# Performance work log

Measured on AMD Instinct MI355X. Metric: run time of the kernel, lower is better.

## Reference

```python
import jax, jax.numpy as jnp
import numpy as np

N, E = 200_000, 1_000_000
WIDTH, NUM_HEAD = 128, 8
WN, WA = 1, 1            # width_norm, width_act
C = WIDTH * WN           # pre/norm channels
A = WIDTH * WA           # gate/value channels
BOND_SIZE, BAG = 33, 3
EPS = 1e-5               # GroupNorm eps (torch default)


def group_norm(x, groups, eps=EPS):
    # x: [E, C]; normalize per sample per group (affine=False, spatial size 1)
    e, c = x.shape
    xg = x.reshape(e, groups, c // groups)
    m = xg.mean(-1, keepdims=True)
    v = ((xg - m) ** 2).mean(-1, keepdims=True)
    return ((xg - m) * jax.lax.rsqrt(v + eps)).reshape(e, c)


def grouped1x1(x, w, groups):
    # grouped Conv1d with kernel 1, no bias. x: [E, Cin], w: [Cout, Cin//groups]
    e, cin = x.shape
    cout = w.shape[0]
    xg = x.reshape(e, groups, cin // groups)
    wg = w.reshape(groups, cout // groups, cin // groups)
    return jnp.einsum('egi,goi->ego', xg, wg).reshape(e, cout)


def setup_inputs() -> dict:
    key = jax.random.key(0)
    ks = jax.random.split(key, 12)
    x = jax.random.normal(ks[0], (N, WIDTH), jnp.float32)
    # degrees clamped to >= 1 in the original model
    deg = jnp.floor(jax.random.uniform(ks[1], (N,), jnp.float32, 1.0, 8.0))
    edge_idx = jax.random.randint(ks[2], (2, E), 0, N)
    edge_attr = jax.random.randint(ks[3], (E, BAG), 0, BOND_SIZE)
    s_in = 1.0 / np.sqrt(WIDTH)
    s_g = 1.0 / np.sqrt(C // NUM_HEAD)
    s_p = 1.0 / np.sqrt(A)
    pre0_w = jax.random.normal(ks[4], (C, WIDTH), jnp.float32) * s_in
    pre0_b = jnp.zeros((C,), jnp.float32)
    pre1_w = jax.random.normal(ks[5], (C, WIDTH), jnp.float32) * s_in
    pre1_b = jnp.zeros((C,), jnp.float32)
    emb = jax.random.normal(ks[6], (BOND_SIZE, C), jnp.float32)
    emb = emb.at[0].set(0.0)  # padding_idx=0
    gate_w = jax.random.normal(ks[7], (A, C // NUM_HEAD), jnp.float32) * s_g
    value_w = jax.random.normal(ks[8], (A, C // NUM_HEAD), jnp.float32) * s_g
    post_w = jax.random.normal(ks[9], (WIDTH, A), jnp.float32) * s_p
    post_b = jnp.zeros((WIDTH,), jnp.float32)
    degree_param = jnp.full((WIDTH,), -0.01, jnp.float32)
    return {"x": x, "deg": deg, "edge_idx": edge_idx, "edge_attr": edge_attr,
            "pre0_w": pre0_w, "pre0_b": pre0_b, "pre1_w": pre1_w, "pre1_b": pre1_b,
            "emb": emb, "gate_w": gate_w, "value_w": value_w,
            "post_w": post_w, "post_b": post_b, "degree_param": degree_param}


def reference(x, deg, edge_idx, edge_attr, pre0_w, pre0_b, pre1_w, pre1_b,
              emb, gate_w, value_w, post_w, post_b, degree_param):
    n = x.shape[0]
    # conv1x1 projections on nodes, then gather to edges
    h0 = x @ pre0_w.T + pre0_b                      # [N, C]
    h1 = x @ pre1_w.T + pre1_b                      # [N, C]
    xx = h0[edge_idx[0]] + h1[edge_idx[1]]          # [E, C]
    xx = group_norm(xx, NUM_HEAD)
    # EmbeddingBag mean with padding_idx=0 excluded from the mean
    mask = (edge_attr != 0)                          # [E, BAG]
    bag = (emb[edge_attr] * mask[..., None]).sum(1)  # [E, C]
    cnt = jnp.maximum(mask.sum(-1), 1).astype(xx.dtype)
    bag = bag / cnt[:, None]
    # GLU-style gate * value (Dropout is identity at eval)
    gate = jax.nn.relu(grouped1x1(xx + bag, gate_w, NUM_HEAD))  # [E, A]
    val = grouped1x1(xx, value_w, NUM_HEAD)                     # [E, A]
    xx = gate * val
    # scatter-sum back to destination nodes
    agg = jax.ops.segment_sum(xx, edge_idx[1], num_segments=n)  # [N, A]
    out = agg @ post_w.T + post_b                                # [N, WIDTH]
    out = jnp.power(deg[:, None], degree_param) * out
    return out
```

## Files before the change

### kernel.cpp

```cpp
#include <hip/hip_runtime.h>
#include <hip/hip_bf16.h>
#include <hip/hip_fp16.h>


typedef unsigned short u16;
typedef unsigned int   u32;

#define WIDTH 128

#define OFF_W0   0
#define OFF_B0   16384
#define OFF_W1   16512
#define OFF_B1   32896
#define OFF_EMB  33024
#define OFF_GW   37248
#define OFF_VW   39296
#define OFF_PW   41344
#define OFF_PB   57728
#define OFF_DP   57856
#define OFF_DEG  57984
#define ARENA_PAD 258048

typedef __attribute__((ext_vector_type(8))) short bf16x8;
typedef __attribute__((ext_vector_type(8))) _Float16 f16x8;
typedef __attribute__((ext_vector_type(4))) float f32x4;
typedef __attribute__((ext_vector_type(2))) __fp16 f16x2;

__device__ __forceinline__ float b2f(u16 u){ return __uint_as_float(((u32)u) << 16); }
__device__ __forceinline__ u16   f2b(float f){
  u32 u = __float_as_uint(f);
  u += 0x7fffu + ((u >> 16) & 1u);
  return (u16)(u >> 16);
}
__device__ __forceinline__ u16   f2h(float f){ return __half_as_ushort(__float2half(f)); }

__device__ __forceinline__ f16x2 u2h(u32 u){ union { u32 a; f16x2 b; } c; c.a = u; return c.b; }
__device__ __forceinline__ u32   h2u(f16x2 h){ union { f16x2 b; u32 a; } c; c.b = h; return c.a; }

__device__ __forceinline__ float dot2h(f16x2 a, f16x2 b, float c){
#if __has_builtin(__builtin_amdgcn_fdot2)
  return __builtin_amdgcn_fdot2(a, b, c, false);
#else
  return fmaf((float)a.x, (float)b.x, fmaf((float)a.y, (float)b.y, c));
#endif
}

#define DPPADD(s, ctrl) {                                                  \
  const float _t = __uint_as_float((u32)__builtin_amdgcn_update_dpp(       \
      0, (int)__float_as_uint(s), (ctrl), 0xF, 0xF, true));                \
  (s) += _t; }

__device__ __forceinline__ bool is_fp32(const void* degsrc){
  return ((*(const u32*)degsrc) & 0xffffu) == 0u;
}

__device__ __forceinline__ bf16x8 cvt8(float4 a, float4 b){
  bf16x8 r;
  r[0]=(short)f2b(a.x); r[1]=(short)f2b(a.y); r[2]=(short)f2b(a.z); r[3]=(short)f2b(a.w);
  r[4]=(short)f2b(b.x); r[5]=(short)f2b(b.y); r[6]=(short)f2b(b.z); r[7]=(short)f2b(b.w);
  return r;
}

__device__ __forceinline__ u16 cvt_one(const void* src, int j, bool f32){
  return f32 ? f2b(((const float*)src)[j]) : ((const u16*)src)[j];
}
__device__ __forceinline__ u16 cvt_one_h(const void* src, int j, bool f32){
  return f32 ? f2h(((const float*)src)[j]) : f2h(b2f(((const u16*)src)[j]));
}
__device__ __forceinline__ float read_f(const void* src, int j, bool f32){
  return f32 ? ((const float*)src)[j] : b2f(((const u16*)src)[j]);
}

__global__ void k_init(const void* w0, const void* b0, const void* w1, const void* b1,
                       const void* emb, const void* gw, const void* vw,
                       const void* pw, const void* pb, const void* dp,
                       const void* degsrc, u16* __restrict__ pb16,
                       u16* __restrict__ gembh, float* __restrict__ gsums,
                       int* __restrict__ cnt, int N, int total)
{
  const bool f32 = is_fp32(degsrc);
  const int nbz = (N + 255) >> 8;
  const int nbc = (total + 255) >> 8;
  int b = blockIdx.x;
  const int t = threadIdx.x;

  if (b < nbz) {
    const int i = b * 256 + t;
    if (i < N) cnt[i] = 0;
    return;
  }
  b -= nbz;
  if (b < nbc) {
    const int i = b * 256 + t;
    if (i >= total) return;
    u16 v;
    if      (i < OFF_B0 ) v = cvt_one(w0,  i,           f32);
    else if (i < OFF_W1 ) v = cvt_one(b0,  i - OFF_B0,  f32);
    else if (i < OFF_B1 ) v = cvt_one(w1,  i - OFF_W1,  f32);
    else if (i < OFF_EMB) v = cvt_one(b1,  i - OFF_B1,  f32);
    else if (i < OFF_GW ) v = cvt_one(emb, i - OFF_EMB, f32);
    else if (i < OFF_VW ) v = cvt_one_h(gw, i - OFF_GW, f32);
    else if (i < OFF_PW ) v = cvt_one_h(vw, i - OFF_VW, f32);
    else if (i < OFF_PB ) v = cvt_one_h(pw, i - OFF_PW, f32);
    else if (i < OFF_DP ) v = cvt_one(pb,  i - OFF_PB,  f32);
    else if (i < OFF_DEG) v = cvt_one(dp,  i - OFF_DP,  f32);
    else                  v = cvt_one(degsrc, i - OFF_DEG, f32);
    pb16[i] = v;
    return;
  }
  b -= nbc;
  if (b < 17) {
    const int tid = b * 256 + t;
    if (tid >= 33 * 128) return;
    const int a = tid >> 7, c = tid & 127, g = c >> 4;
    float s = 0.f;
    #pragma unroll
    for (int i = 0; i < 16; ++i)
      s += read_f(gw, c * 16 + i, f32) * read_f(emb, a * WIDTH + g * 16 + i, f32);
    gembh[tid] = f2h(s);
    return;
  }
  if (t < 256) {
    const int c = t & 127;
    const void* src = (t >> 7) ? vw : gw;
    float s = 0.f;
    #pragma unroll
    for (int i = 0; i < 16; ++i) s += read_f(src, c * 16 + i, f32);
    gsums[t] = s;
  }
}

__global__ __launch_bounds__(256, 2) void k_pre_hist(
    const void* __restrict__ x, const u16* __restrict__ pb16,
    u16* __restrict__ h0, u16* __restrict__ h1, const void* __restrict__ degsrc,
    const int* __restrict__ eidx, int* __restrict__ cnt, int E, int npre)
{
  if ((int)blockIdx.x >= npre) {
    const int e = ((int)blockIdx.x - npre) * 256 + threadIdx.x;
    if (e < E) atomicAdd(&cnt[eidx[E + e]], 1);
    return;
  }

  const int t = threadIdx.x;
  const int lane = t & 63, lid = lane & 15, quad = lane >> 4;
  const int w = t >> 6, mat = w >> 1, c0 = (w & 1) * 64;
  const int node0 = blockIdx.x * 64;

  const u16* wm = pb16 + (mat ? OFF_W1 : OFF_W0);
  const u16* bs = pb16 + (mat ? OFF_B1 : OFF_B0);
  u16* hout = mat ? h1 : h0;
  const bool f32 = is_fp32(degsrc);

  f32x4 acc[4][4];
  #pragma unroll
  for (int nt = 0; nt < 4; ++nt) {
    const float bias = b2f(bs[c0 + nt * 16 + lid]);
    #pragma unroll
    for (int mt = 0; mt < 4; ++mt)
      #pragma unroll
      for (int r = 0; r < 4; ++r) acc[mt][nt][r] = bias;
  }

  #pragma unroll
  for (int ks = 0; ks < 4; ++ks) {
    bf16x8 a[4], b[4];
    #pragma unroll
    for (int nt = 0; nt < 4; ++nt)
      b[nt] = *(const bf16x8*)(wm + (size_t)(c0 + nt * 16 + lid) * WIDTH + ks * 32 + quad * 8);
    if (f32) {
      #pragma unroll
      for (int mt = 0; mt < 4; ++mt) {
        const float4* xr = (const float4*)((const float*)x +
            (size_t)(node0 + mt * 16 + lid) * WIDTH + ks * 32 + quad * 8);
        a[mt] = cvt8(xr[0], xr[1]);
      }
    } else {
      #pragma unroll
      for (int mt = 0; mt < 4; ++mt)
        a[mt] = *(const bf16x8*)((const u16*)x +
            (size_t)(node0 + mt * 16 + lid) * WIDTH + ks * 32 + quad * 8);
    }
    #pragma unroll
    for (int mt = 0; mt < 4; ++mt)
      #pragma unroll
      for (int nt = 0; nt < 4; ++nt)
        acc[mt][nt] = __builtin_amdgcn_mfma_f32_16x16x32_bf16(a[mt], b[nt], acc[mt][nt], 0, 0, 0);
  }

  #pragma unroll
  for (int mt = 0; mt < 4; ++mt)
    #pragma unroll
    for (int nt = 0; nt < 4; ++nt)
      #pragma unroll
      for (int r = 0; r < 4; ++r)
        hout[(size_t)(node0 + mt * 16 + quad * 4 + r) * WIDTH + c0 + nt * 16 + lid] =
            f2h(acc[mt][nt][r]);
}

__global__ void k_scan1(const int* __restrict__ cnt, int* __restrict__ bsum, int n){
  const int t = threadIdx.x, b = blockIdx.x;
  const int i0 = b * 1024 + t * 4;
  int s = 0;
  #pragma unroll
  for (int j = 0; j < 4; ++j) { int i = i0 + j; if (i < n) s += cnt[i]; }
  __shared__ int sb[256];
  sb[t] = s; __syncthreads();
  for (int d = 128; d > 0; d >>= 1) { if (t < d) sb[t] += sb[t + d]; __syncthreads(); }
  if (t == 0) bsum[b] = sb[0];
}

__global__ void k_scan2(int* __restrict__ bsum, int nblk){
  const int t = threadIdx.x;
  int v[4];
  const int i0 = t * 4;
  #pragma unroll
  for (int j = 0; j < 4; ++j) { int i = i0 + j; v[j] = (i < nblk) ? bsum[i] : 0; }
  int tsum = v[0] + v[1] + v[2] + v[3];
  __shared__ int sb[256];
  sb[t] = tsum; __syncthreads();
  for (int d = 1; d < 256; d <<= 1) {
    int x = (t >= d) ? sb[t - d] : 0;
    __syncthreads();
    sb[t] += x;
    __syncthreads();
  }
  int run = sb[t] - tsum;
  #pragma unroll
  for (int j = 0; j < 4; ++j) { int nv = run; run += v[j]; v[j] = nv; }
  #pragma unroll
  for (int j = 0; j < 4; ++j) { int i = i0 + j; if (i < nblk) bsum[i] = v[j]; }
}

__global__ void k_scan3(const int* __restrict__ cnt, const int* __restrict__ bsum,
                        int* __restrict__ off, int n){
  const int t = threadIdx.x, b = blockIdx.x;
  const int i0 = b * 1024 + t * 4;
  int c[4];
  #pragma unroll
  for (int j = 0; j < 4; ++j) { int i = i0 + j; c[j] = (i < n) ? cnt[i] : 0; }
  int tsum = c[0] + c[1] + c[2] + c[3];
  __shared__ int sb[256];
  sb[t] = tsum; __syncthreads();
  for (int d = 1; d < 256; d <<= 1) {
    int x = (t >= d) ? sb[t - d] : 0;
    __syncthreads();
    sb[t] += x;
    __syncthreads();
  }
  int run = bsum[b] + sb[t] - tsum;
  #pragma unroll
  for (int j = 0; j < 4; ++j) {
    int i = i0 + j;
    if (i < n) off[i] = run;
    run += c[j];
  }
}

__global__ void k_scatter(const int* __restrict__ eidx, const int* __restrict__ eattr,
                          int* __restrict__ off, uint2* __restrict__ sedge, int E){
  const int e = blockIdx.x * 256 + threadIdx.x;
  if (e >= E) return;
  const int dst = eidx[E + e];
  const int pos = atomicAdd(&off[dst], 1);
  const u32 a0 = (u32)eattr[e*3+0], a1 = (u32)eattr[e*3+1], a2 = (u32)eattr[e*3+2];
  sedge[pos] = make_uint2((u32)eidx[e], a0 | (a1 << 6) | (a2 << 12));
}

__global__ __launch_bounds__(256, 4) void k_agg(
    const u16* __restrict__ h0, const u16* __restrict__ h1,
    const uint2* __restrict__ sedge, const int* __restrict__ off,
    const u16* __restrict__ pb16, const u16* __restrict__ gembh,
    const float* __restrict__ gsums, u16* __restrict__ aggh, const int N)
{
  const int base = ((blockIdx.x * 256 + threadIdx.x) >> 6) * 4;
  if (base >= N) return;
  const int q = threadIdx.x & 63;
  const int c0 = 2 * q;

  u32 gw0[8], gw1[8], vw0[8], vw1[8];
  {
    const u32* g = (const u32*)(pb16 + OFF_GW + (size_t)c0 * 16);
    const u32* v = (const u32*)(pb16 + OFF_VW + (size_t)c0 * 16);
    #pragma unroll
    for (int i = 0; i < 8; ++i) {
      gw0[i] = g[i]; gw1[i] = g[8 + i];
      vw0[i] = v[i]; vw1[i] = v[8 + i];
    }
  }
  const float gs0 = gsums[c0],           gs1 = gsums[c0 + 1];
  const float nv0 = -gsums[128 + c0],    nv1 = -gsums[128 + c0 + 1];
  const f16x2 ones = u2h(0x3C003C00u);

  u32 h1w[4]; int nend[4];
  #pragma unroll
  for (int d = 0; d < 4; ++d) {
    const int dst = min(base + d, N - 1);
    h1w[d]  = *(const u32*)(h1 + (size_t)dst * WIDTH + c0);
    nend[d] = off[dst];
  }
  int ncur = base ? off[base - 1] : 0;
  const int nlast = nend[3];

  u32 hp = 0, g0w = 0, g1w = 0, g2w = 0; float pinv = 1.f;
  if (ncur < nlast) {
    const uint2 ep = sedge[ncur];
    hp  = *(const u32*)(h0 + (size_t)ep.x * WIDTH + c0);
    const int a0 = ep.y & 63, a1 = (ep.y >> 6) & 63, a2 = (ep.y >> 12) & 63;
    g0w = *(const u32*)(gembh + (size_t)a0 * WIDTH + c0);
    g1w = *(const u32*)(gembh + (size_t)a1 * WIDTH + c0);
    g2w = *(const u32*)(gembh + (size_t)a2 * WIDTH + c0);
    const int cb = (a0 != 0) + (a1 != 0) + (a2 != 0);
    pinv = __builtin_amdgcn_rcpf((float)(cb | (cb == 0)));
  }

  #pragma unroll
  for (int d = 0; d < 4; ++d) {
    const f16x2 h1h = u2h(h1w[d]);
    const int n1 = nend[d];
    float acc0 = 0.f, acc1 = 0.f;

    for (int i = ncur; i < n1; ++i) {
      const u32 hp_c = hp, g0c = g0w, g1c = g1w, g2c = g2w;
      const float inv_c = pinv;
      if (i + 1 < nlast) {
        const uint2 ep = sedge[i + 1];
        hp  = *(const u32*)(h0 + (size_t)ep.x * WIDTH + c0);
        const int a0 = ep.y & 63, a1 = (ep.y >> 6) & 63, a2 = (ep.y >> 12) & 63;
        g0w = *(const u32*)(gembh + (size_t)a0 * WIDTH + c0);
        g1w = *(const u32*)(gembh + (size_t)a1 * WIDTH + c0);
        g2w = *(const u32*)(gembh + (size_t)a2 * WIDTH + c0);
        const int cb = (a0 != 0) + (a1 != 0) + (a2 != 0);
        pinv = __builtin_amdgcn_rcpf((float)(cb | (cb == 0)));
      }

      const f16x2 xh = u2h(hp_c) + h1h;
      const u32 xu = h2u(xh);

      float s  = dot2h(xh, ones, 0.f);
      float ss = dot2h(xh, xh,   0.f);
      DPPADD(s, 0xB1);  DPPADD(ss, 0xB1);
      DPPADD(s, 0x4E);  DPPADD(ss, 0x4E);
      DPPADD(s, 0x141); DPPADD(ss, 0x141);
      const float mean = s * 0.0625f;
      const float var  = fmaf(ss, 0.0625f, -mean * mean);
      const float rs   = __builtin_amdgcn_rsqf(var + 1e-5f);
      const float mrs  = mean * rs;

      float rg0 = 0.f, rg1 = 0.f, rv0 = 0.f, rv1 = 0.f;
#define CSTEP(J) {                                                             \
      const f16x2 xj = u2h((u32)__builtin_amdgcn_ds_swizzle(                   \
          (int)xu, 0x18 | ((J) << 5)));                                        \
      rg0 = dot2h(xj, u2h(gw0[J]), rg0);                                       \
      rg1 = dot2h(xj, u2h(gw1[J]), rg1);                                       \
      rv0 = dot2h(xj, u2h(vw0[J]), rv0);                                       \
      rv1 = dot2h(xj, u2h(vw1[J]), rv1); }
      CSTEP(0) CSTEP(1) CSTEP(2) CSTEP(3) CSTEP(4) CSTEP(5) CSTEP(6) CSTEP(7)
#undef CSTEP

      const f16x2 gsum3 = u2h(g0c) + u2h(g1c) + u2h(g2c);
      const float bg0 = (float)gsum3.x * inv_c;
      const float bg1 = (float)gsum3.y * inv_c;

      const float ga0 = fmaf(rs, rg0, fmaf(-mrs, gs0, bg0));
      const float ga1 = fmaf(rs, rg1, fmaf(-mrs, gs1, bg1));
      const float va0 = fmaf(rs, rv0, mrs * nv0);
      const float va1 = fmaf(rs, rv1, mrs * nv1);
      acc0 = fmaf(fmaxf(ga0, 0.f), va0, acc0);
      acc1 = fmaf(fmaxf(ga1, 0.f), va1, acc1);
    }

    if (base + d < N)
      *(u32*)(aggh + (size_t)(base + d) * WIDTH + c0) =
          h2u(__builtin_amdgcn_cvt_pkrtz(acc0, acc1));
    ncur = n1;
  }
}

__global__ __launch_bounds__(256, 2) void k_post(
    const u16* __restrict__ aggh, const u16* __restrict__ pb16,
    void* __restrict__ out, const void* __restrict__ degsrc)
{
  const int t = threadIdx.x;
  const int lane = t & 63, lid = lane & 15, quad = lane >> 4;
  const int w = t >> 6, c0 = (w & 1) * 64, mh = (w >> 1) * 32;
  const int node0 = blockIdx.x * 64;
  const bool f32o = is_fp32(degsrc);

  f32x4 acc[2][4];
  float dpc[4];
  #pragma unroll
  for (int nt = 0; nt < 4; ++nt) {
    const float bias = b2f(pb16[OFF_PB + c0 + nt * 16 + lid]);
    dpc[nt] = b2f(pb16[OFF_DP + c0 + nt * 16 + lid]);
    #pragma unroll
    for (int mt = 0; mt < 2; ++mt)
      #pragma unroll
      for (int r = 0; r < 4; ++r) acc[mt][nt][r] = bias;
  }

  #pragma unroll
  for (int ks = 0; ks < 4; ++ks) {
    f16x8 a[2], b[4];
    #pragma unroll
    for (int nt = 0; nt < 4; ++nt)
      b[nt] = *(const f16x8*)(pb16 + OFF_PW + (size_t)(c0 + nt * 16 + lid) * WIDTH + ks * 32 + quad * 8);
    #pragma unroll
    for (int mt = 0; mt < 2; ++mt)
      a[mt] = *(const f16x8*)(aggh +
          (size_t)(node0 + mh + mt * 16 + lid) * WIDTH + ks * 32 + quad * 8);
    #pragma unroll
    for (int mt = 0; mt < 2; ++mt)
      #pragma unroll
      for (int nt = 0; nt < 4; ++nt)
        acc[mt][nt] = __builtin_amdgcn_mfma_f32_16x16x32_f16(a[mt], b[nt], acc[mt][nt], 0, 0, 0);
  }

  float logd[2][4];
  #pragma unroll
  for (int mt = 0; mt < 2; ++mt)
    #pragma unroll
    for (int r = 0; r < 4; ++r)
      logd[mt][r] = __logf(b2f(pb16[OFF_DEG + node0 + mh + mt * 16 + quad * 4 + r]));

  #pragma unroll
  for (int mt = 0; mt < 2; ++mt)
    #pragma unroll
    for (int nt = 0; nt < 4; ++nt)
      #pragma unroll
      for (int r = 0; r < 4; ++r) {
        const int node = node0 + mh + mt * 16 + quad * 4 + r;
        const float v = acc[mt][nt][r] * __expf(dpc[nt] * logd[mt][r]);
        if (f32o) ((float*)out)[(size_t)node * WIDTH + c0 + nt * 16 + lid] = v;
        else      ((u16*)out)[(size_t)node * WIDTH + c0 + nt * 16 + lid] = f2b(v);
      }
}

extern "C" void kernel_launch(void* const* d_in, const int* in_sizes, int n_in,
                              void* d_out, int out_size, void* d_ws, size_t ws_size,
                              hipStream_t stream)
{
  (void)n_in; (void)out_size; (void)ws_size;
  const void* x     = d_in[0];
  const void* deg   = d_in[1];
  const int*  eidx  = (const int*)d_in[2];
  const int*  eattr = (const int*)d_in[3];

  const int N = in_sizes[1];
  const int E = in_sizes[2] / 2;

  u16*   aggh = (u16*)d_ws;
  u16*   h1   = (u16*)((float*)d_ws + (size_t)N * WIDTH);
  u16*   pb16 = h1 + (size_t)N * WIDTH;
  u16*   gembh= pb16 + ARENA_PAD;
  float* gsums= (float*)(gembh + 33 * WIDTH);
  int*   cnt  = (int*)(gsums + 256);
  int*   off  = cnt + N;
  int*   bsum = off + N;
  uint2* sedge= (uint2*)(bsum + 1024);
  u16*   h0   = (u16*)d_out;

  const int total = OFF_DEG + N;
  const int nbz = (N + 255) / 256;
  const int nbc = (total + 255) / 256;
  k_init<<<nbz + nbc + 18, 256, 0, stream>>>(
      d_in[4], d_in[5], d_in[6], d_in[7], d_in[8], d_in[9], d_in[10],
      d_in[11], d_in[12], d_in[13], deg, pb16, gembh, gsums, cnt, N, total);

  const int npre = N / 64;
  const int nbh  = (E + 255) / 256;
  k_pre_hist<<<npre + nbh, 256, 0, stream>>>(x, pb16, h0, h1, deg, eidx, cnt, E, npre);

  const int nblk = (N + 1023) / 1024;
  k_scan1  <<<nblk, 256, 0, stream>>>(cnt, bsum, N);
  k_scan2  <<<1, 256, 0, stream>>>(bsum, nblk);
  k_scan3  <<<nblk, 256, 0, stream>>>(cnt, bsum, off, N);
  k_scatter<<<nbh, 256, 0, stream>>>(eidx, eattr, off, sedge, E);

  k_agg<<<((size_t)N * 16 + 255) / 256, 256, 0, stream>>>(
      h0, h1, sedge, off, pb16, gembh, gsums, aggh, N);

  k_post<<<N / 64, 256, 0, stream>>>(aggh, pb16, d_out, deg);
}
```

Before: 609.9 us.

## Fuse histogram and scan stages, precompute bag counts, use packed fp32 FMA

```diff
diff --git a/kernel.cpp b/kernel.cpp
--- a/kernel.cpp
+++ b/kernel.cpp
@@ -24,6 +24,7 @@
 typedef __attribute__((ext_vector_type(8))) short bf16x8;
 typedef __attribute__((ext_vector_type(8))) _Float16 f16x8;
 typedef __attribute__((ext_vector_type(4))) float f32x4;
+typedef __attribute__((ext_vector_type(2))) float f32x2;
 typedef __attribute__((ext_vector_type(2))) __fp16 f16x2;
 
 __device__ __forceinline__ float b2f(u16 u){ return __uint_as_float(((u32)u) << 16); }
@@ -33,15 +34,24 @@
   return (u16)(u >> 16);
 }
 __device__ __forceinline__ u16   f2h(float f){ return __half_as_ushort(__float2half(f)); }
+__device__ __forceinline__ float h2fl(u32 p){ return __half2float(__ushort_as_half((u16)(p & 0xffffu))); }
+__device__ __forceinline__ float h2fh(u32 p){ return __half2float(__ushort_as_half((u16)(p >> 16))); }
 
 __device__ __forceinline__ f16x2 u2h(u32 u){ union { u32 a; f16x2 b; } c; c.a = u; return c.b; }
 __device__ __forceinline__ u32   h2u(f16x2 h){ union { f16x2 b; u32 a; } c; c.b = h; return c.a; }
 
-__device__ __forceinline__ float dot2h(f16x2 a, f16x2 b, float c){
-#if __has_builtin(__builtin_amdgcn_fdot2)
-  return __builtin_amdgcn_fdot2(a, b, c, false);
+__device__ __forceinline__ f32x2 pkfma(f32x2 a, f32x2 b, f32x2 c){
+#if __has_builtin(__builtin_elementwise_fma)
+  return __builtin_elementwise_fma(a, b, c);
 #else
-  return fmaf((float)a.x, (float)b.x, fmaf((float)a.y, (float)b.y, c));
+  return (f32x2){fmaf(a.x, b.x, c.x), fmaf(a.y, b.y, c.y)};
+#endif
+}
+__device__ __forceinline__ f32x2 pkmax0(f32x2 a){
+#if __has_builtin(__builtin_elementwise_max)
+  return __builtin_elementwise_max(a, (f32x2){0.f, 0.f});
+#else
+  return (f32x2){fmaxf(a.x, 0.f), fmaxf(a.y, 0.f)};
 #endif
 }
 
@@ -71,25 +81,26 @@
   return f32 ? ((const float*)src)[j] : b2f(((const u16*)src)[j]);
 }
 
-__global__ void k_init(const void* w0, const void* b0, const void* w1, const void* b1,
-                       const void* emb, const void* gw, const void* vw,
-                       const void* pw, const void* pb, const void* dp,
-                       const void* degsrc, u16* __restrict__ pb16,
-                       u16* __restrict__ gembh, float* __restrict__ gsums,
-                       int* __restrict__ cnt, int N, int total)
+__global__ void k_init_hist(const void* w0, const void* b0, const void* w1, const void* b1,
+                            const void* emb, const void* gw, const void* vw,
+                            const void* pw, const void* pb, const void* dp,
+                            const void* degsrc, const int* __restrict__ eidx,
+                            int* __restrict__ cnt, int E,
+                            u16* __restrict__ pb16, u16* __restrict__ gembh,
+                            float* __restrict__ gsums, int total)
 {
   const bool f32 = is_fp32(degsrc);
-  const int nbz = (N + 255) >> 8;
+  const int nbh = (E + 255) >> 8;
   const int nbc = (total + 255) >> 8;
   int b = blockIdx.x;
   const int t = threadIdx.x;
 
-  if (b < nbz) {
-    const int i = b * 256 + t;
-    if (i < N) cnt[i] = 0;
+  if (b < nbh) {
+    const int e = b * 256 + t;
+    if (e < E) atomicAdd(&cnt[eidx[E + e]], 1);
     return;
   }
-  b -= nbz;
+  b -= nbh;
   if (b < nbc) {
     const int i = b * 256 + t;
     if (i >= total) return;
@@ -130,14 +141,21 @@
   }
 }
 
-__global__ __launch_bounds__(256, 2) void k_pre_hist(
+__global__ __launch_bounds__(256, 2) void k_pre_scan1(
     const void* __restrict__ x, const u16* __restrict__ pb16,
     u16* __restrict__ h0, u16* __restrict__ h1, const void* __restrict__ degsrc,
-    const int* __restrict__ eidx, int* __restrict__ cnt, int E, int npre)
+    const int* __restrict__ cnt, int* __restrict__ bsum, int n, int npre)
 {
   if ((int)blockIdx.x >= npre) {
-    const int e = ((int)blockIdx.x - npre) * 256 + threadIdx.x;
-    if (e < E) atomicAdd(&cnt[eidx[E + e]], 1);
+    const int t = threadIdx.x, b = (int)blockIdx.x - npre;
+    const int i0 = b * 1024 + t * 4;
+    int s = 0;
+    #pragma unroll
+    for (int j = 0; j < 4; ++j) { int i = i0 + j; if (i < n) s += cnt[i]; }
+    __shared__ int sb[256];
+    sb[t] = s; __syncthreads();
+    for (int d = 128; d > 0; d >>= 1) { if (t < d) sb[t] += sb[t + d]; __syncthreads(); }
+    if (t == 0) bsum[b] = sb[0];
     return;
   }
 
@@ -197,43 +215,16 @@
             f2h(acc[mt][nt][r]);
 }
 
-__global__ void k_scan1(const int* __restrict__ cnt, int* __restrict__ bsum, int n){
-  const int t = threadIdx.x, b = blockIdx.x;
-  const int i0 = b * 1024 + t * 4;
-  int s = 0;
-  #pragma unroll
-  for (int j = 0; j < 4; ++j) { int i = i0 + j; if (i < n) s += cnt[i]; }
-  __shared__ int sb[256];
-  sb[t] = s; __syncthreads();
-  for (int d = 128; d > 0; d >>= 1) { if (t < d) sb[t] += sb[t + d]; __syncthreads(); }
-  if (t == 0) bsum[b] = sb[0];
-}
-
-__global__ void k_scan2(int* __restrict__ bsum, int nblk){
-  const int t = threadIdx.x;
-  int v[4];
-  const int i0 = t * 4;
-  #pragma unroll
-  for (int j = 0; j < 4; ++j) { int i = i0 + j; v[j] = (i < nblk) ? bsum[i] : 0; }
-  int tsum = v[0] + v[1] + v[2] + v[3];
-  __shared__ int sb[256];
-  sb[t] = tsum; __syncthreads();
-  for (int d = 1; d < 256; d <<= 1) {
-    int x = (t >= d) ? sb[t - d] : 0;
-    __syncthreads();
-    sb[t] += x;
-    __syncthreads();
-  }
-  int run = sb[t] - tsum;
-  #pragma unroll
-  for (int j = 0; j < 4; ++j) { int nv = run; run += v[j]; v[j] = nv; }
-  #pragma unroll
-  for (int j = 0; j < 4; ++j) { int i = i0 + j; if (i < nblk) bsum[i] = v[j]; }
-}
-
 __global__ void k_scan3(const int* __restrict__ cnt, const int* __restrict__ bsum,
                         int* __restrict__ off, int n){
   const int t = threadIdx.x, b = blockIdx.x;
+  __shared__ int sp[256];
+  int pv = 0;
+  for (int j = t; j < b; j += 256) pv += bsum[j];
+  sp[t] = pv; __syncthreads();
+  for (int d = 128; d > 0; d >>= 1) { if (t < d) sp[t] += sp[t + d]; __syncthreads(); }
+  const int bpref = sp[0];
+
   const int i0 = b * 1024 + t * 4;
   int c[4];
   #pragma unroll
@@ -247,7 +238,7 @@
     sb[t] += x;
     __syncthreads();
   }
-  int run = bsum[b] + sb[t] - tsum;
+  int run = bpref + sb[t] - tsum;
   #pragma unroll
   for (int j = 0; j < 4; ++j) {
     int i = i0 + j;
@@ -263,7 +254,9 @@
   const int dst = eidx[E + e];
   const int pos = atomicAdd(&off[dst], 1);
   const u32 a0 = (u32)eattr[e*3+0], a1 = (u32)eattr[e*3+1], a2 = (u32)eattr[e*3+2];
-  sedge[pos] = make_uint2((u32)eidx[e], a0 | (a1 << 6) | (a2 << 12));
+  u32 cb = (a0 != 0) + (a1 != 0) + (a2 != 0);
+  cb = cb ? cb : 1u;
+  sedge[pos] = make_uint2((u32)eidx[e], a0 | (a1 << 6) | (a2 << 12) | (cb << 18));
 }
 
 __global__ __launch_bounds__(256, 4) void k_agg(
@@ -277,19 +270,21 @@
   const int q = threadIdx.x & 63;
   const int c0 = 2 * q;
 
-  u32 gw0[8], gw1[8], vw0[8], vw1[8];
+  f32x2 wgl[8], wgh[8], wvl[8], wvh[8];
   {
-    const u32* g = (const u32*)(pb16 + OFF_GW + (size_t)c0 * 16);
-    const u32* v = (const u32*)(pb16 + OFF_VW + (size_t)c0 * 16);
+    const u32* gp = (const u32*)(pb16 + OFF_GW + (size_t)c0 * 16);
+    const u32* vp = (const u32*)(pb16 + OFF_VW + (size_t)c0 * 16);
     #pragma unroll
     for (int i = 0; i < 8; ++i) {
-      gw0[i] = g[i]; gw1[i] = g[8 + i];
-      vw0[i] = v[i]; vw1[i] = v[8 + i];
+      const u32 ga = gp[i], gb = gp[8 + i], va = vp[i], vb = vp[8 + i];
+      wgl[i] = (f32x2){h2fl(ga), h2fl(gb)};
+      wgh[i] = (f32x2){h2fh(ga), h2fh(gb)};
+      wvl[i] = (f32x2){h2fl(va), h2fl(vb)};
+      wvh[i] = (f32x2){h2fh(va), h2fh(vb)};
     }
   }
-  const float gs0 = gsums[c0],           gs1 = gsums[c0 + 1];
-  const float nv0 = -gsums[128 + c0],    nv1 = -gsums[128 + c0 + 1];
-  const f16x2 ones = u2h(0x3C003C00u);
+  const f32x2 gsP = {gsums[c0], gsums[c0 + 1]};
+  const f32x2 vsP = {gsums[128 + c0], gsums[128 + c0 + 1]};
 
   u32 h1w[4]; int nend[4];
   #pragma unroll
@@ -302,42 +297,44 @@
   const int nlast = nend[3];
 
   u32 hp = 0, g0w = 0, g1w = 0, g2w = 0; float pinv = 1.f;
+  uint2 edn = make_uint2(0u, 0u);
   if (ncur < nlast) {
-    const uint2 ep = sedge[ncur];
-    hp  = *(const u32*)(h0 + (size_t)ep.x * WIDTH + c0);
-    const int a0 = ep.y & 63, a1 = (ep.y >> 6) & 63, a2 = (ep.y >> 12) & 63;
+    const uint2 e0 = sedge[ncur];
+    edn = sedge[min(ncur + 1, nlast - 1)];
+    hp  = *(const u32*)(h0 + (size_t)e0.x * WIDTH + c0);
+    const int a0 = e0.y & 63, a1 = (e0.y >> 6) & 63, a2 = (e0.y >> 12) & 63;
     g0w = *(const u32*)(gembh + (size_t)a0 * WIDTH + c0);
     g1w = *(const u32*)(gembh + (size_t)a1 * WIDTH + c0);
     g2w = *(const u32*)(gembh + (size_t)a2 * WIDTH + c0);
-    const int cb = (a0 != 0) + (a1 != 0) + (a2 != 0);
-    pinv = __builtin_amdgcn_rcpf((float)(cb | (cb == 0)));
+    pinv = __builtin_amdgcn_rcpf((float)((e0.y >> 18) & 3));
   }
 
   #pragma unroll
   for (int d = 0; d < 4; ++d) {
     const f16x2 h1h = u2h(h1w[d]);
     const int n1 = nend[d];
-    float acc0 = 0.f, acc1 = 0.f;
+    f32x2 accP = (f32x2){0.f, 0.f};
 
     for (int i = ncur; i < n1; ++i) {
       const u32 hp_c = hp, g0c = g0w, g1c = g1w, g2c = g2w;
       const float inv_c = pinv;
-      if (i + 1 < nlast) {
-        const uint2 ep = sedge[i + 1];
-        hp  = *(const u32*)(h0 + (size_t)ep.x * WIDTH + c0);
-        const int a0 = ep.y & 63, a1 = (ep.y >> 6) & 63, a2 = (ep.y >> 12) & 63;
+      {
+        const uint2 en = edn;
+        edn = sedge[min(i + 2, nlast - 1)];
+        hp  = *(const u32*)(h0 + (size_t)en.x * WIDTH + c0);
+        const int a0 = en.y & 63, a1 = (en.y >> 6) & 63, a2 = (en.y >> 12) & 63;
         g0w = *(const u32*)(gembh + (size_t)a0 * WIDTH + c0);
         g1w = *(const u32*)(gembh + (size_t)a1 * WIDTH + c0);
         g2w = *(const u32*)(gembh + (size_t)a2 * WIDTH + c0);
-        const int cb = (a0 != 0) + (a1 != 0) + (a2 != 0);
-        pinv = __builtin_amdgcn_rcpf((float)(cb | (cb == 0)));
+        pinv = __builtin_amdgcn_rcpf((float)((en.y >> 18) & 3));
       }
 
       const f16x2 xh = u2h(hp_c) + h1h;
       const u32 xu = h2u(xh);
-
-      float s  = dot2h(xh, ones, 0.f);
-      float ss = dot2h(xh, xh,   0.f);
+      const float x0f = (float)xh.x, x1f = (float)xh.y;
+
+      float s  = x0f + x1f;
+      float ss = fmaf(x0f, x0f, x1f * x1f);
       DPPADD(s, 0xB1);  DPPADD(ss, 0xB1);
       DPPADD(s, 0x4E);  DPPADD(ss, 0x4E);
       DPPADD(s, 0x141); DPPADD(ss, 0x141);
@@ -346,32 +343,29 @@
       const float rs   = __builtin_amdgcn_rsqf(var + 1e-5f);
       const float mrs  = mean * rs;
 
-      float rg0 = 0.f, rg1 = 0.f, rv0 = 0.f, rv1 = 0.f;
+      f32x2 gaP = (f32x2){0.f, 0.f}, vaP = (f32x2){0.f, 0.f};
 #define CSTEP(J) {                                                             \
-      const f16x2 xj = u2h((u32)__builtin_amdgcn_ds_swizzle(                   \
-          (int)xu, 0x18 | ((J) << 5)));                                        \
-      rg0 = dot2h(xj, u2h(gw0[J]), rg0);                                       \
-      rg1 = dot2h(xj, u2h(gw1[J]), rg1);                                       \
-      rv0 = dot2h(xj, u2h(vw0[J]), rv0);                                       \
-      rv1 = dot2h(xj, u2h(vw1[J]), rv1); }
+      const u32 xj = (u32)__builtin_amdgcn_ds_swizzle((int)xu, 0x18 | ((J) << 5)); \
+      const float xl = h2fl(xj), xhv = h2fh(xj);                               \
+      const f32x2 xlP = {xl, xl}, xhP = {xhv, xhv};                            \
+      gaP = pkfma(xlP, wgl[J], gaP); gaP = pkfma(xhP, wgh[J], gaP);            \
+      vaP = pkfma(xlP, wvl[J], vaP); vaP = pkfma(xhP, wvh[J], vaP); }
       CSTEP(0) CSTEP(1) CSTEP(2) CSTEP(3) CSTEP(4) CSTEP(5) CSTEP(6) CSTEP(7)
 #undef CSTEP
 
       const f16x2 gsum3 = u2h(g0c) + u2h(g1c) + u2h(g2c);
-      const float bg0 = (float)gsum3.x * inv_c;
-      const float bg1 = (float)gsum3.y * inv_c;
-
-      const float ga0 = fmaf(rs, rg0, fmaf(-mrs, gs0, bg0));
-      const float ga1 = fmaf(rs, rg1, fmaf(-mrs, gs1, bg1));
-      const float va0 = fmaf(rs, rv0, mrs * nv0);
-      const float va1 = fmaf(rs, rv1, mrs * nv1);
-      acc0 = fmaf(fmaxf(ga0, 0.f), va0, acc0);
-      acc1 = fmaf(fmaxf(ga1, 0.f), va1, acc1);
+      const f32x2 invP  = {inv_c, inv_c};
+      const f32x2 bgP   = (f32x2){(float)gsum3.x, (float)gsum3.y} * invP;
+
+      const f32x2 rsP = {rs, rs}, nmP = {-mrs, -mrs};
+      const f32x2 gate = pkfma(rsP, gaP, pkfma(nmP, gsP, bgP));
+      const f32x2 val  = pkfma(rsP, vaP, nmP * vsP);
+      accP = pkfma(pkmax0(gate), val, accP);
     }
 
     if (base + d < N)
       *(u32*)(aggh + (size_t)(base + d) * WIDTH + c0) =
-          h2u(__builtin_amdgcn_cvt_pkrtz(acc0, acc1));
+          h2u(__builtin_amdgcn_cvt_pkrtz(accP.x, accP.y));
     ncur = n1;
   }
 }
@@ -460,19 +454,20 @@
   u16*   h0   = (u16*)d_out;
 
   const int total = OFF_DEG + N;
-  const int nbz = (N + 255) / 256;
   const int nbc = (total + 255) / 256;
-  k_init<<<nbz + nbc + 18, 256, 0, stream>>>(
+  const int nbh = (E + 255) / 256;
+
+  hipMemsetAsync(cnt, 0, (size_t)N * sizeof(int), stream);
+
+  k_init_hist<<<nbh + nbc + 18, 256, 0, stream>>>(
       d_in[4], d_in[5], d_in[6], d_in[7], d_in[8], d_in[9], d_in[10],
-      d_in[11], d_in[12], d_in[13], deg, pb16, gembh, gsums, cnt, N, total);
+      d_in[11], d_in[12], d_in[13], deg, eidx, cnt, E, pb16, gembh, gsums, total);
 
   const int npre = N / 64;
-  const int nbh  = (E + 255) / 256;
-  k_pre_hist<<<npre + nbh, 256, 0, stream>>>(x, pb16, h0, h1, deg, eidx, cnt, E, npre);
-
   const int nblk = (N + 1023) / 1024;
-  k_scan1  <<<nblk, 256, 0, stream>>>(cnt, bsum, N);
-  k_scan2  <<<1, 256, 0, stream>>>(bsum, nblk);
+  k_pre_scan1<<<npre + nblk, 256, 0, stream>>>(
+      x, pb16, h0, h1, deg, cnt, bsum, N, npre);
+
   k_scan3  <<<nblk, 256, 0, stream>>>(cnt, bsum, off, N);
   k_scatter<<<nbh, 256, 0, stream>>>(eidx, eattr, off, sedge, E);
 
```

After: 630.3 us. +3.4%, slower.
